# Performance work log

Hardware: AMD Instinct MI355X
Metric: run time of the kernel (lower is better)

## Reference

```python
import jax, jax.numpy as jnp
import numpy as np
import math

MH_C = 2.0 / (math.sqrt(3.0) * math.pi ** 0.25)  # mexican hat normalization

def setup_inputs() -> dict:
    key = jax.random.key(0)
    ks = jax.random.split(key, 4)
    B, O, I, H, W = 4, 32, 32, 128, 128
    x = jax.random.normal(ks[0], (B, I, H, W), dtype=jnp.float32)
    scale_param = jnp.ones((1, O, I, 1, 1), dtype=jnp.float32)
    translation_param = jax.random.normal(ks[1], (1, O, I, 1, 1), dtype=jnp.float32)
    wavelet_conv_w = jax.random.normal(ks[2], (O, I, 3, 3), dtype=jnp.float32) * (1.0 / math.sqrt(I * 9))
    final_conv_w = jax.random.normal(ks[3], (O, O, 1, 1), dtype=jnp.float32) * (1.0 / math.sqrt(O))
    return {"x": x, "scale_param": scale_param, "translation_param": translation_param,
            "wavelet_conv_w": wavelet_conv_w, "final_conv_w": final_conv_w}

def reference(x, scale_param, translation_param, wavelet_conv_w, final_conv_w):
    # x: (B, I, H, W) -> scaled: (B, O, I, H, W)
    sx = (x[:, None] - translation_param) / scale_param
    # mexican hat wavelet, fused elementwise
    wt = MH_C * ((sx * sx - 1.0) * jnp.exp(-0.5 * sx * sx))
    B, O, I, H, W = wt.shape
    # The per-out-channel loop of Conv2d(I,1,k) is exactly a grouped conv with O groups
    wt = wt.reshape(B, O * I, H, W)
    y = jax.lax.conv_general_dilated(
        wt, wavelet_conv_w,
        window_strides=(1, 1), padding=[(1, 1), (1, 1)],
        feature_group_count=O,
        dimension_numbers=("NCHW", "OIHW", "NCHW"))  # (B, O, H, W)
    # final 1x1 conv = channel mix
    out = jnp.einsum("oc,bchw->bohw", final_conv_w[:, :, 0, 0], y)
    return out
```

## Files before the change

### kernel.cpp

```cpp
#include <hip/hip_runtime.h>
#include <math.h>


#define RSTRIP 8

typedef float v2f __attribute__((ext_vector_type(2)));

static __device__ __forceinline__ v2f vfma(float w, v2f a, v2f c) {
  return __builtin_elementwise_fma(a, (v2f){w, w}, c);
}
static __device__ __forceinline__ float bperm(int addr, float v) {
  return __int_as_float(__builtin_amdgcn_ds_bpermute(addr, __float_as_int(v)));
}
static __device__ __forceinline__ v2f psi2(v2f xv, float rs, float trs, float m) {
  const float NHL2E = -0.72134752044448170f;
  const v2f sx = __builtin_elementwise_fma(xv, (v2f){rs, rs}, (v2f){-trs, -trs});
  const v2f u  = sx * sx;
  v2f e;
  e.x = __builtin_amdgcn_exp2f(u.x * NHL2E);
  e.y = __builtin_amdgcn_exp2f(u.y * NHL2E);
  return __builtin_elementwise_fma(u, (v2f){m, m}, (v2f){-m, -m}) * e;
}

#define LDROW(base, r) (*(const v2f*)((base) + (size_t)(min(max((r), 0), 127)) * 128))

__global__ __launch_bounds__(256) void wavelet_grouped_conv(
    const float* __restrict__ x,
    const float* __restrict__ scale,
    const float* __restrict__ trans,
    const float* __restrict__ wconv,
    float* __restrict__ y,
    float mhc)
{
  const int tid   = threadIdx.x;
  const int lane  = tid & 63;
  const int iq    = tid >> 6;
  const int strip = blockIdx.x;
  const int o     = blockIdx.y;
  const int b     = blockIdx.z;
  const int r0    = strip * RSTRIP;
  const int c0    = lane << 1;

  const int a_up = ((lane + 63) & 63) << 2;
  const int a_dn = ((lane +  1) & 63) << 2;
  const bool lane0  = (lane == 0);
  const bool lane63 = (lane == 63);

  const float mhc_m1 = (r0 > 0)       ? mhc : 0.f;
  const float mhc_p8 = (r0 + 8 < 128) ? mhc : 0.f;

  v2f TL[RSTRIP], TC[RSTRIP], TR[RSTRIP];
#pragma unroll
  for (int r = 0; r < RSTRIP; ++r) {
    TL[r] = (v2f){0.f, 0.f}; TC[r] = (v2f){0.f, 0.f}; TR[r] = (v2f){0.f, 0.f};
  }

  const float* xb = x + (size_t)b * 32 * 128 * 128;
  const int oibase = __builtin_amdgcn_readfirstlane(o * 32 + iq * 8);

#define CHBASE(k) (xb + (size_t)(min(iq * 8 + (k), 31)) * 128 * 128 + c0)

#define CHANNEL(BUF, NBUF, K)                                               \
  {                                                                         \
    const int oi = oibase + (K);                                            \
    const float rs  = 1.0f / scale[oi];                                     \
    const float trs = trans[oi] * rs;                                       \
    const float* wp = wconv + oi * 9;                                       \
    const float w00 = wp[0], w01 = wp[1], w02 = wp[2];                      \
    const float w10 = wp[3], w11 = wp[4], w12 = wp[5];                      \
    const float w20 = wp[6], w21 = wp[7], w22 = wp[8];                      \
    const float* nb = CHBASE((K) + 1);                                      \
    _Pragma("unroll")                                                       \
    for (int k = 0; k < RSTRIP + 2; ++k) NBUF[k] = LDROW(nb, r0 + k - 1);   \
    _Pragma("unroll")                                                       \
    for (int j = 0; j < RSTRIP + 2; ++j) {                                  \
      const float mj = (j == 0) ? mhc_m1 : (j == RSTRIP + 1) ? mhc_p8 : mhc;\
      const v2f p = psi2(BUF[j], rs, trs, mj);                              \
      if (j <= RSTRIP - 1) {                                                \
        TL[j] = vfma(w00, p, TL[j]);                                        \
        TC[j] = vfma(w01, p, TC[j]);                                        \
        TR[j] = vfma(w02, p, TR[j]);                                        \
      }                                                                     \
      if (j >= 1 && j <= RSTRIP) {                                          \
        TL[j-1] = vfma(w10, p, TL[j-1]);                                    \
        TC[j-1] = vfma(w11, p, TC[j-1]);                                    \
        TR[j-1] = vfma(w12, p, TR[j-1]);                                    \
      }                                                                     \
      if (j >= 2) {                                                         \
        TL[j-2] = vfma(w20, p, TL[j-2]);                                    \
        TC[j-2] = vfma(w21, p, TC[j-2]);                                    \
        TR[j-2] = vfma(w22, p, TR[j-2]);                                    \
      }                                                                     \
    }                                                                       \
  }

  v2f bufA[RSTRIP + 2], bufB[RSTRIP + 2];
  {
    const float* b0 = CHBASE(0);
#pragma unroll
    for (int k = 0; k < RSTRIP + 2; ++k) bufA[k] = LDROW(b0, r0 + k - 1);
  }

#pragma unroll 1
  for (int ii = 0; ii < 4; ++ii) {
    CHANNEL(bufA, bufB, 2 * ii)
    CHANNEL(bufB, bufA, 2 * ii + 1)
  }
#undef CHANNEL
#undef CHBASE

  v2f acc[RSTRIP];
#pragma unroll
  for (int r = 0; r < RSTRIP; ++r) {
    float pl = bperm(a_up, TL[r].y);
    float pr = bperm(a_dn, TR[r].x);
    if (lane0)  pl = 0.f;
    if (lane63) pr = 0.f;
    v2f v;
    v.x = pl      + TC[r].x + TR[r].y;
    v.y = TL[r].x + TC[r].y + pr;
    acc[r] = v;
  }

  __shared__ v2f red[3][RSTRIP][64];
  if (iq != 0) {
#pragma unroll
    for (int r = 0; r < RSTRIP; ++r) red[iq - 1][r][lane] = acc[r];
  }
  __syncthreads();
  if (iq == 0) {
    float* yb = y + (((size_t)b * 32 + o) * 128 + r0) * 128 + c0;
#pragma unroll
    for (int r = 0; r < RSTRIP; ++r) {
      const v2f v = acc[r] + red[0][r][lane] + red[1][r][lane] + red[2][r][lane];
      *(v2f*)(yb + (size_t)r * 128) = v;
    }
  }
}

__global__ __launch_bounds__(256) void mix1x1(
    const float* __restrict__ y,
    const float* __restrict__ fw,
    float* __restrict__ out)
{
  const int px = blockIdx.x * 256 + threadIdx.x;
  const int b  = blockIdx.y;
  const float* yb = y + (size_t)b * 32 * 16384 + px;
  float v[32];
#pragma unroll
  for (int o = 0; o < 32; ++o) v[o] = yb[(size_t)o * 16384];
  float* ob = out + (size_t)b * 32 * 16384 + px;
#pragma unroll
  for (int p = 0; p < 32; ++p) {
    float a = 0.f;
#pragma unroll
    for (int o = 0; o < 32; ++o) a = fmaf(fw[p * 32 + o], v[o], a);
    ob[(size_t)p * 16384] = a;
  }
}

extern "C" void kernel_launch(void* const* d_in, const int* in_sizes, int n_in,
                              void* d_out, int out_size, void* d_ws, size_t ws_size,
                              hipStream_t stream) {
  const float* x     = (const float*)d_in[0];
  const float* scale = (const float*)d_in[1];
  const float* trans = (const float*)d_in[2];
  const float* wconv = (const float*)d_in[3];
  const float* fw    = (const float*)d_in[4];
  float* out = (float*)d_out;
  float* y   = (float*)d_ws;

  const float mhc = (float)(2.0 / (sqrt(3.0) * pow(M_PI, 0.25)));

  dim3 g1(128 / RSTRIP, 32, 4);
  wavelet_grouped_conv<<<g1, 256, 0, stream>>>(x, scale, trans, wconv, y, mhc);

  dim3 g2(16384 / 256, 4);
  mix1x1<<<g2, 256, 0, stream>>>(y, fw, out);
}
```

Baseline: 48.45 us.

## Share staged input rows across 8 output channels via async LDS double buffering

```diff
diff --git a/kernel.cpp b/kernel.cpp
--- a/kernel.cpp
+++ b/kernel.cpp
@@ -21,10 +21,13 @@
   e.y = __builtin_amdgcn_exp2f(u.y * NHL2E);
   return __builtin_elementwise_fma(u, (v2f){m, m}, (v2f){-m, -m}) * e;
 }
-
-#define LDROW(base, r) (*(const v2f*)((base) + (size_t)(min(max((r), 0), 127)) * 128))
-
-__global__ __launch_bounds__(256) void wavelet_grouped_conv(
+static __device__ __forceinline__ void gload_lds16(const float* g, float* l) {
+  __builtin_amdgcn_global_load_lds(
+      (const __attribute__((address_space(1))) void*)g,
+      (__attribute__((address_space(3))) void*)l, 16, 0, 0);
+}
+
+__global__ __launch_bounds__(1024) void wavelet_grouped_conv(
     const float* __restrict__ x,
     const float* __restrict__ scale,
     const float* __restrict__ trans,
@@ -34,10 +37,13 @@
 {
   const int tid   = threadIdx.x;
   const int lane  = tid & 63;
-  const int iq    = tid >> 6;
+  const int w     = tid >> 6;
+  const int o_idx = w & 7;
+  const int ihalf = w >> 3;
   const int strip = blockIdx.x;
-  const int o     = blockIdx.y;
+  const int og    = blockIdx.y;
   const int b     = blockIdx.z;
+  const int o     = og * 8 + o_idx;
   const int r0    = strip * RSTRIP;
   const int c0    = lane << 1;
 
@@ -56,58 +62,74 @@
   }
 
   const float* xb = x + (size_t)b * 32 * 128 * 128;
-  const int oibase = __builtin_amdgcn_readfirstlane(o * 32 + iq * 8);
-
-#define CHBASE(k) (xb + (size_t)(min(iq * 8 + (k), 31)) * 128 * 128 + c0)
-
-#define CHANNEL(BUF, NBUF, K)                                               \
+
+  __shared__ float stage[2][5120];
+
+#define STAGE(bufp, c)                                                  \
+  {                                                                     \
+    _Pragma("unroll")                                                   \
+    for (int t = 0; t < 2; ++t) {                                       \
+      const int s = w + t * 16;                                         \
+      if (s < 20) {                                                     \
+        const int ch = s / 5, rp = s % 5;                               \
+        const int row = 2 * rp + (lane >> 5);                           \
+        const int ir  = min(max(r0 + row - 1, 0), 127);                 \
+        const float* g = xb + (size_t)((c) * 4 + ch) * 16384            \
+                            + ir * 128 + (lane & 31) * 4;               \
+        gload_lds16(g, (bufp) + s * 256);                               \
+      }                                                                 \
+    }                                                                   \
+  }
+
+#define COMPUTE(bufp, c)                                                    \
   {                                                                         \
-    const int oi = oibase + (K);                                            \
-    const float rs  = 1.0f / scale[oi];                                     \
-    const float trs = trans[oi] * rs;                                       \
-    const float* wp = wconv + oi * 9;                                       \
-    const float w00 = wp[0], w01 = wp[1], w02 = wp[2];                      \
-    const float w10 = wp[3], w11 = wp[4], w12 = wp[5];                      \
-    const float w20 = wp[6], w21 = wp[7], w22 = wp[8];                      \
-    const float* nb = CHBASE((K) + 1);                                      \
     _Pragma("unroll")                                                       \
-    for (int k = 0; k < RSTRIP + 2; ++k) NBUF[k] = LDROW(nb, r0 + k - 1);   \
-    _Pragma("unroll")                                                       \
-    for (int j = 0; j < RSTRIP + 2; ++j) {                                  \
-      const float mj = (j == 0) ? mhc_m1 : (j == RSTRIP + 1) ? mhc_p8 : mhc;\
-      const v2f p = psi2(BUF[j], rs, trs, mj);                              \
-      if (j <= RSTRIP - 1) {                                                \
-        TL[j] = vfma(w00, p, TL[j]);                                        \
-        TC[j] = vfma(w01, p, TC[j]);                                        \
-        TR[j] = vfma(w02, p, TR[j]);                                        \
-      }                                                                     \
-      if (j >= 1 && j <= RSTRIP) {                                          \
-        TL[j-1] = vfma(w10, p, TL[j-1]);                                    \
-        TC[j-1] = vfma(w11, p, TC[j-1]);                                    \
-        TR[j-1] = vfma(w12, p, TR[j-1]);                                    \
-      }                                                                     \
-      if (j >= 2) {                                                         \
-        TL[j-2] = vfma(w20, p, TL[j-2]);                                    \
-        TC[j-2] = vfma(w21, p, TC[j-2]);                                    \
-        TR[j-2] = vfma(w22, p, TR[j-2]);                                    \
+    for (int cl = 0; cl < 2; ++cl) {                                        \
+      const int chl = 2 * ihalf + cl;                                       \
+      const int oi = __builtin_amdgcn_readfirstlane(o * 32 + (c) * 4 + chl);\
+      const float rs  = 1.0f / scale[oi];                                   \
+      const float trs = trans[oi] * rs;                                     \
+      const float* wp = wconv + oi * 9;                                     \
+      const float w00 = wp[0], w01 = wp[1], w02 = wp[2];                    \
+      const float w10 = wp[3], w11 = wp[4], w12 = wp[5];                    \
+      const float w20 = wp[6], w21 = wp[7], w22 = wp[8];                    \
+      const float* xs = (bufp) + chl * 1280 + c0;                           \
+      _Pragma("unroll")                                                     \
+      for (int j = 0; j < RSTRIP + 2; ++j) {                                \
+        const float mj = (j == 0) ? mhc_m1 : (j == RSTRIP + 1) ? mhc_p8 : mhc;\
+        const v2f p = psi2(*(const v2f*)(xs + j * 128), rs, trs, mj);       \
+        if (j <= RSTRIP - 1) {                                              \
+          TL[j] = vfma(w00, p, TL[j]);                                      \
+          TC[j] = vfma(w01, p, TC[j]);                                      \
+          TR[j] = vfma(w02, p, TR[j]);                                      \
+        }                                                                   \
+        if (j >= 1 && j <= RSTRIP) {                                        \
+          TL[j-1] = vfma(w10, p, TL[j-1]);                                  \
+          TC[j-1] = vfma(w11, p, TC[j-1]);                                  \
+          TR[j-1] = vfma(w12, p, TR[j-1]);                                  \
+        }                                                                   \
+        if (j >= 2) {                                                       \
+          TL[j-2] = vfma(w20, p, TL[j-2]);                                  \
+          TC[j-2] = vfma(w21, p, TC[j-2]);                                  \
+          TR[j-2] = vfma(w22, p, TR[j-2]);                                  \
+        }                                                                   \
       }                                                                     \
     }                                                                       \
   }
 
-  v2f bufA[RSTRIP + 2], bufB[RSTRIP + 2];
-  {
-    const float* b0 = CHBASE(0);
-#pragma unroll
-    for (int k = 0; k < RSTRIP + 2; ++k) bufA[k] = LDROW(b0, r0 + k - 1);
-  }
+  STAGE(stage[0], 0)
+  asm volatile("s_waitcnt vmcnt(0)" ::: "memory");
+  __syncthreads();
 
 #pragma unroll 1
-  for (int ii = 0; ii < 4; ++ii) {
-    CHANNEL(bufA, bufB, 2 * ii)
-    CHANNEL(bufB, bufA, 2 * ii + 1)
-  }
-#undef CHANNEL
-#undef CHBASE
+  for (int c = 0; c < 8; ++c) {
+    if (c < 7) STAGE(stage[(c + 1) & 1], c + 1)
+    COMPUTE(stage[c & 1], c)
+    asm volatile("s_waitcnt vmcnt(0)" ::: "memory");
+    __syncthreads();
+  }
+#undef COMPUTE
+#undef STAGE
 
   v2f acc[RSTRIP];
 #pragma unroll
@@ -122,17 +144,18 @@
     acc[r] = v;
   }
 
-  __shared__ v2f red[3][RSTRIP][64];
-  if (iq != 0) {
-#pragma unroll
-    for (int r = 0; r < RSTRIP; ++r) red[iq - 1][r][lane] = acc[r];
+  float* red = &stage[0][0];
+  if (ihalf == 1) {
+#pragma unroll
+    for (int r = 0; r < RSTRIP; ++r)
+      *(v2f*)(red + ((o_idx * RSTRIP + r) * 64 + lane) * 2) = acc[r];
   }
   __syncthreads();
-  if (iq == 0) {
+  if (ihalf == 0) {
     float* yb = y + (((size_t)b * 32 + o) * 128 + r0) * 128 + c0;
 #pragma unroll
     for (int r = 0; r < RSTRIP; ++r) {
-      const v2f v = acc[r] + red[0][r][lane] + red[1][r][lane] + red[2][r][lane];
+      const v2f v = acc[r] + *(const v2f*)(red + ((o_idx * RSTRIP + r) * 64 + lane) * 2);
       *(v2f*)(yb + (size_t)r * 128) = v;
     }
   }
@@ -172,8 +195,8 @@
 
   const float mhc = (float)(2.0 / (sqrt(3.0) * pow(M_PI, 0.25)));
 
-  dim3 g1(128 / RSTRIP, 32, 4);
-  wavelet_grouped_conv<<<g1, 256, 0, stream>>>(x, scale, trans, wconv, y, mhc);
+  dim3 g1(16, 4, 4);
+  wavelet_grouped_conv<<<g1, 1024, 0, stream>>>(x, scale, trans, wconv, y, mhc);
 
   dim3 g2(16384 / 256, 4);
   mix1x1<<<g2, 256, 0, stream>>>(y, fw, out);
```

Result: faster. 46.29 us (-4.5%).

## Stage input rows into LDS via direct global-to-LDS loads with double buffering

Applied to the files above, without the earlier changes.

```diff
diff --git a/kernel.cpp b/kernel.cpp
--- a/kernel.cpp
+++ b/kernel.cpp
@@ -21,8 +21,11 @@
   e.y = __builtin_amdgcn_exp2f(u.y * NHL2E);
   return __builtin_elementwise_fma(u, (v2f){m, m}, (v2f){-m, -m}) * e;
 }
-
-#define LDROW(base, r) (*(const v2f*)((base) + (size_t)(min(max((r), 0), 127)) * 128))
+static __device__ __forceinline__ void gload_lds16(const float* g, float* l) {
+  __builtin_amdgcn_global_load_lds(
+      (const __attribute__((address_space(1))) void*)g,
+      (__attribute__((address_space(3))) void*)l, 16, 0, 0);
+}
 
 __global__ __launch_bounds__(256) void wavelet_grouped_conv(
     const float* __restrict__ x,
@@ -56,26 +59,39 @@
   }
 
   const float* xb = x + (size_t)b * 32 * 128 * 128;
-  const int oibase = __builtin_amdgcn_readfirstlane(o * 32 + iq * 8);
-
-#define CHBASE(k) (xb + (size_t)(min(iq * 8 + (k), 31)) * 128 * 128 + c0)
-
-#define CHANNEL(BUF, NBUF, K)                                               \
+
+  __shared__ float stage[4][2][1280];
+  float* base0 = &stage[iq][0][0];
+
+  int goff[5];
+#pragma unroll
+  for (int k = 0; k < 5; ++k) {
+    int row = r0 - 1 + 2 * k + (lane >> 5);
+    row = min(max(row, 0), 127);
+    goff[k] = row * 128 + (lane & 31) * 4;
+  }
+
+#define STAGE_CH(bufp, K)                                          \
+  {                                                                \
+    const float* xch = xb + (size_t)(iq * 8 + (K)) * 16384;        \
+    _Pragma("unroll")                                              \
+    for (int k = 0; k < 5; ++k)                                    \
+      gload_lds16(xch + goff[k], (bufp) + k * 256);                \
+  }
+
+#define COMPUTE(bufp, K)                                                    \
   {                                                                         \
-    const int oi = oibase + (K);                                            \
+    const int oi = __builtin_amdgcn_readfirstlane(o * 32 + iq * 8 + (K));   \
     const float rs  = 1.0f / scale[oi];                                     \
     const float trs = trans[oi] * rs;                                       \
     const float* wp = wconv + oi * 9;                                       \
     const float w00 = wp[0], w01 = wp[1], w02 = wp[2];                      \
     const float w10 = wp[3], w11 = wp[4], w12 = wp[5];                      \
     const float w20 = wp[6], w21 = wp[7], w22 = wp[8];                      \
-    const float* nb = CHBASE((K) + 1);                                      \
-    _Pragma("unroll")                                                       \
-    for (int k = 0; k < RSTRIP + 2; ++k) NBUF[k] = LDROW(nb, r0 + k - 1);   \
     _Pragma("unroll")                                                       \
     for (int j = 0; j < RSTRIP + 2; ++j) {                                  \
       const float mj = (j == 0) ? mhc_m1 : (j == RSTRIP + 1) ? mhc_p8 : mhc;\
-      const v2f p = psi2(BUF[j], rs, trs, mj);                              \
+      const v2f p = psi2(*(const v2f*)((bufp) + j * 128 + c0), rs, trs, mj);\
       if (j <= RSTRIP - 1) {                                                \
         TL[j] = vfma(w00, p, TL[j]);                                        \
         TC[j] = vfma(w01, p, TC[j]);                                        \
@@ -94,20 +110,24 @@
     }                                                                       \
   }
 
-  v2f bufA[RSTRIP + 2], bufB[RSTRIP + 2];
-  {
-    const float* b0 = CHBASE(0);
-#pragma unroll
-    for (int k = 0; k < RSTRIP + 2; ++k) bufA[k] = LDROW(b0, r0 + k - 1);
-  }
+  STAGE_CH(base0, 0)
 
 #pragma unroll 1
-  for (int ii = 0; ii < 4; ++ii) {
-    CHANNEL(bufA, bufB, 2 * ii)
-    CHANNEL(bufB, bufA, 2 * ii + 1)
-  }
-#undef CHANNEL
-#undef CHBASE
+  for (int c = 0; c < 8; ++c) {
+    float* cur = base0 + (c & 1) * 1280;
+    float* nxt = base0 + ((c + 1) & 1) * 1280;
+    __builtin_amdgcn_sched_barrier(0);
+    if (c < 7) {
+      STAGE_CH(nxt, c + 1)
+      asm volatile("s_waitcnt vmcnt(5)" ::: "memory");
+    } else {
+      asm volatile("s_waitcnt vmcnt(0)" ::: "memory");
+    }
+    __builtin_amdgcn_sched_barrier(0);
+    COMPUTE(cur, c)
+  }
+#undef COMPUTE
+#undef STAGE_CH
 
   v2f acc[RSTRIP];
 #pragma unroll
@@ -122,17 +142,22 @@
     acc[r] = v;
   }
 
-  __shared__ v2f red[3][RSTRIP][64];
+  __syncthreads();
+  float* red = &stage[0][0][0];
   if (iq != 0) {
 #pragma unroll
-    for (int r = 0; r < RSTRIP; ++r) red[iq - 1][r][lane] = acc[r];
+    for (int r = 0; r < RSTRIP; ++r)
+      *(v2f*)(red + (((iq - 1) * RSTRIP + r) * 64 + lane) * 2) = acc[r];
   }
   __syncthreads();
   if (iq == 0) {
     float* yb = y + (((size_t)b * 32 + o) * 128 + r0) * 128 + c0;
 #pragma unroll
     for (int r = 0; r < RSTRIP; ++r) {
-      const v2f v = acc[r] + red[0][r][lane] + red[1][r][lane] + red[2][r][lane];
+      const v2f v = acc[r]
+        + *(const v2f*)(red + ((0 * RSTRIP + r) * 64 + lane) * 2)
+        + *(const v2f*)(red + ((1 * RSTRIP + r) * 64 + lane) * 2)
+        + *(const v2f*)(red + ((2 * RSTRIP + r) * 64 + lane) * 2);
       *(v2f*)(yb + (size_t)r * 128) = v;
     }
   }
@@ -172,7 +197,7 @@
 
   const float mhc = (float)(2.0 / (sqrt(3.0) * pow(M_PI, 0.25)));
 
-  dim3 g1(128 / RSTRIP, 32, 4);
+  dim3 g1(16, 32, 4);
   wavelet_grouped_conv<<<g1, 256, 0, stream>>>(x, scale, trans, wconv, y, mhc);
 
   dim3 g2(16384 / 256, 4);
```

Measured after the change: 47.55 us. About the same (-1.9%).
